# Optimization experiments

Hardware: AMD Instinct MI355X
Metric: run time of the kernel (lower is better)

Reference implementation:

```python
import jax, jax.numpy as jnp
import numpy as np

N_NODES = 50000
N_EDGES = 500000
CLIP_DIM = 512   # openai/clip-vit-base-patch32 projection_dim
HIDDEN = 512
NUM_CLASSES = 100


def setup_inputs() -> dict:
    key = jax.random.key(0)
    ks = jax.random.split(key, 8)
    x = jax.random.normal(ks[0], (N_NODES, CLIP_DIM), dtype=jnp.float32)
    edge_index = jax.random.randint(ks[1], (2, N_EDGES), 0, N_NODES)
    W1 = jax.random.normal(ks[2], (HIDDEN, CLIP_DIM), dtype=jnp.float32) / np.sqrt(CLIP_DIM)
    b1 = jnp.zeros((HIDDEN,), dtype=jnp.float32)
    W2 = jax.random.normal(ks[3], (HIDDEN, HIDDEN), dtype=jnp.float32) / np.sqrt(HIDDEN)
    b2 = jnp.zeros((HIDDEN,), dtype=jnp.float32)
    Wc = jax.random.normal(ks[4], (NUM_CLASSES, HIDDEN), dtype=jnp.float32) / np.sqrt(HIDDEN)
    bc = jnp.zeros((NUM_CLASSES,), dtype=jnp.float32)
    return {"x": x, "edge_index": edge_index, "W1": W1, "b1": b1,
            "W2": W2, "b2": b2, "Wc": Wc, "bc": bc}


def _gcn_conv(h, W, b, src, dst, coef, n_nodes):
    # PyG GCNConv: transform, then normalized scatter-add aggregation, then bias.
    h = h @ W.T                                   # [N, out]
    msg = h[src] * coef[:, None]                  # [E+N, out] gathered messages
    out = jax.ops.segment_sum(msg, dst, num_segments=n_nodes)
    return out + b


def reference(x, edge_index, W1, b1, W2, b2, Wc, bc):
    n = x.shape[0]
    loop = jnp.arange(n, dtype=edge_index.dtype)
    src = jnp.concatenate([edge_index[0], loop])  # add self-loops (GCN default)
    dst = jnp.concatenate([edge_index[1], loop])
    # symmetric normalization deg^-1/2 on both endpoints (unit edge weights)
    deg = jax.ops.segment_sum(jnp.ones_like(src, dtype=x.dtype), dst, num_segments=n)
    norm = jax.lax.rsqrt(deg)                     # deg >= 1 due to self-loops
    coef = norm[src] * norm[dst]

    h = _gcn_conv(x, W1, b1, src, dst, coef, n)
    h = jax.nn.relu(h)
    # dropout(p=0.2) is identity in eval mode
    h = _gcn_conv(h, W2, b2, src, dst, coef, n)
    h = jax.nn.relu(h)
    return h @ Wc.T + bc                          # [N, num_classes]
```

## Files before the change

### kernel.cpp

```cpp
#include <hip/hip_runtime.h>

#define HIDDEN 512
#define BLK_ELEMS (64 * 128 * 8)

typedef __attribute__((ext_vector_type(8))) short short8;
typedef __attribute__((ext_vector_type(4))) float f32x4;

__device__ __forceinline__ unsigned short f2bf(float f) {
    unsigned u = __float_as_uint(f);
    unsigned r = (u + 0x7FFFu + ((u >> 16) & 1u)) >> 16;
    return (unsigned short)r;
}
__device__ __forceinline__ float bf2f(unsigned short h) {
    return __uint_as_float(((unsigned)h) << 16);
}

__device__ __forceinline__ void load_lds16(const unsigned short* g, unsigned short* l) {
    __builtin_amdgcn_global_load_lds(
        (const __attribute__((address_space(1))) unsigned int*)(g),
        (__attribute__((address_space(3))) unsigned int*)(l), 16, 0, 0);
}

__device__ __forceinline__ void acc8(uint4 v, float cf, float* a) {
    a[0] = fmaf(cf, bf2f((unsigned short)(v.x & 0xFFFF)), a[0]);
    a[1] = fmaf(cf, bf2f((unsigned short)(v.x >> 16)),    a[1]);
    a[2] = fmaf(cf, bf2f((unsigned short)(v.y & 0xFFFF)), a[2]);
    a[3] = fmaf(cf, bf2f((unsigned short)(v.y >> 16)),    a[3]);
    a[4] = fmaf(cf, bf2f((unsigned short)(v.z & 0xFFFF)), a[4]);
    a[5] = fmaf(cf, bf2f((unsigned short)(v.z >> 16)),    a[5]);
    a[6] = fmaf(cf, bf2f((unsigned short)(v.w & 0xFFFF)), a[6]);
    a[7] = fmaf(cf, bf2f((unsigned short)(v.w >> 16)),    a[7]);
}


__device__ __forceinline__ void cast_chunk(const float* __restrict__ src,
                                           unsigned short* __restrict__ dst,
                                           int rows, int o) {
    int blk = o >> 13;
    int rem = o & 8191;
    int g = rem >> 7;
    int m = rem & 127;
    int row = blk * 128 + m;
    short8 v;
    if (row < rows) {
        const float* p = src + (size_t)row * HIDDEN + g * 8;
        float4 f0 = *(const float4*)p;
        float4 f1 = *(const float4*)(p + 4);
        v[0] = (short)f2bf(f0.x); v[1] = (short)f2bf(f0.y);
        v[2] = (short)f2bf(f0.z); v[3] = (short)f2bf(f0.w);
        v[4] = (short)f2bf(f1.x); v[5] = (short)f2bf(f1.y);
        v[6] = (short)f2bf(f1.z); v[7] = (short)f2bf(f1.w);
    } else {
        v = (short8)0;
    }
    *(short8*)(dst + (size_t)o * 8) = v;
}


__global__ __launch_bounds__(256)
void fused_count_castx(const int* __restrict__ dstv, int* __restrict__ cnt, int E, int countB,
                       const float* __restrict__ x, unsigned short* __restrict__ bufA,
                       int rows, int nxb) {
    int b = blockIdx.x;
    if (b < countB) {
        int e = b * 256 + threadIdx.x;
        if (e < E) atomicAdd(&cnt[dstv[e]], 1);
        return;
    }
    int cb = b - countB;
    if (cb >= nxb) return;
    __shared__ __align__(16) unsigned short xs[32 * 520];
    const int tid = threadIdx.x;
    const int r0 = cb * 32;
    #pragma unroll
    for (int p = 0; p < 16; ++p) {
        int f = p * 1024 + tid * 4;
        int rl = f >> 9;
        int col = f & 511;
        int grow = r0 + rl;
        uint2 w = make_uint2(0u, 0u);
        if (grow < rows) {
            float4 v = *(const float4*)(x + (size_t)grow * HIDDEN + col);
            w.x = (unsigned)f2bf(v.x) | ((unsigned)f2bf(v.y) << 16);
            w.y = (unsigned)f2bf(v.z) | ((unsigned)f2bf(v.w) << 16);
        }
        *(uint2*)(xs + rl * 520 + col) = w;
    }
    __syncthreads();
    const int blk = r0 >> 7;
    const int m0 = r0 & 127;
    unsigned short* dstb = bufA + (size_t)blk * BLK_ELEMS;
    #pragma unroll
    for (int p = 0; p < 8; ++p) {
        int c = p * 256 + tid;
        int g = c >> 5;
        int mloc = c & 31;
        short8 v = *(const short8*)(xs + mloc * 520 + g * 8);
        *(short8*)(dstb + g * 1024 + (m0 + mloc) * 8) = v;
    }
}


__global__ __launch_bounds__(256)
void fused_bsum_castw(const int* __restrict__ cnt, float* __restrict__ norm,
                      int* __restrict__ bsums, int n, int NSB,
                      const float* __restrict__ W1, const float* __restrict__ W2,
                      const float* __restrict__ Wc,
                      unsigned short* __restrict__ W1t, unsigned short* __restrict__ W2t,
                      unsigned short* __restrict__ Wct, int NC) {
    __shared__ int red[256];
    int tid = threadIdx.x;
    if ((int)blockIdx.x < NSB) {
        int i = blockIdx.x * 256 + tid;
        int v = 0;
        if (i < n) {
            v = cnt[i];
            norm[i] = rsqrtf((float)(v + 1));
        }
        red[tid] = v;
        __syncthreads();
        #pragma unroll
        for (int off = 128; off > 0; off >>= 1) {
            if (tid < off) red[tid] += red[tid + off];
            __syncthreads();
        }
        if (tid == 0) bsums[blockIdx.x] = red[0];
    } else {
        int o = ((int)blockIdx.x - NSB) * 256 + tid;
        if (o < 32768) {
            cast_chunk(W1, W1t, HIDDEN, o);
        } else if (o < 65536) {
            cast_chunk(W2, W2t, HIDDEN, o - 32768);
        } else if (o < 73728) {
            cast_chunk(Wc, Wct, NC, o - 65536);
        }
    }
}

__global__ __launch_bounds__(256)
void bscan_kernel(const int* __restrict__ bsums, int* __restrict__ boffs,
                  int* __restrict__ rowptr_n, int nb) {
    __shared__ int buf[256];
    int tid = threadIdx.x;
    int v = (tid < nb) ? bsums[tid] : 0;
    buf[tid] = v;
    __syncthreads();
    #pragma unroll
    for (int off = 1; off < 256; off <<= 1) {
        int t = (tid >= off) ? buf[tid - off] : 0;
        __syncthreads();
        buf[tid] += t;
        __syncthreads();
    }
    if (tid < nb) boffs[tid] = buf[tid] - v;
    if (tid == 255) rowptr_n[0] = buf[255];
}

__global__ __launch_bounds__(256)
void scan_final_kernel(const int* __restrict__ cnt, const int* __restrict__ boffs,
                       int* __restrict__ rowptr, int* __restrict__ cursor, int n) {
    __shared__ int buf[256];
    int tid = threadIdx.x;
    int i = blockIdx.x * 256 + tid;
    int v = (i < n) ? cnt[i] : 0;
    buf[tid] = v;
    __syncthreads();
    #pragma unroll
    for (int off = 1; off < 256; off <<= 1) {
        int t = (tid >= off) ? buf[tid - off] : 0;
        __syncthreads();
        buf[tid] += t;
        __syncthreads();
    }
    if (i < n) {
        int ex = boffs[blockIdx.x] + buf[tid] - v;
        rowptr[i] = ex;
        cursor[i] = ex;
    }
}


template<int MODE>
__device__ __forceinline__ void gemm_body(const unsigned short* __restrict__ At,
                                          const unsigned short* __restrict__ Bt,
                                          const float* __restrict__ bias,
                                          void* __restrict__ Cout,
                                          int M, int NC, int mb, int nb) {
    __shared__ __align__(16) unsigned short As[8 * 128 * 8];
    __shared__ __align__(16) unsigned short Bs[8 * 128 * 8];

    const int tid = threadIdx.x;
    const int wid = tid >> 6;
    const int lane = tid & 63;
    const int wm = wid & 1, wn = wid >> 1;
    const int lm = lane & 15;
    const int lq = lane >> 4;

    const unsigned short* Ab = At + (size_t)mb * BLK_ELEMS;
    const unsigned short* Bb = Bt + (size_t)nb * BLK_ELEMS;

    f32x4 acc[4][4];
    #pragma unroll
    for (int i = 0; i < 4; ++i)
        #pragma unroll
        for (int j = 0; j < 4; ++j) acc[i][j] = (f32x4)0.f;

    for (int kt = 0; kt < 8; ++kt) {
        __syncthreads();
        const unsigned short* ga = Ab + kt * (8 * 1024);
        const unsigned short* gb = Bb + kt * (8 * 1024);
        #pragma unroll
        for (int i = 0; i < 4; ++i) {
            int off = (tid + i * 256) * 8;
            load_lds16(ga + off, As + off);
            load_lds16(gb + off, Bs + off);
        }
        __syncthreads();
        #pragma unroll
        for (int ks = 0; ks < 2; ++ks) {
            int g = ks * 4 + lq;
            int base = g * 1024 + lm * 8;
            short8 af[4], bfr[4];
            #pragma unroll
            for (int mt = 0; mt < 4; ++mt)
                af[mt] = *(const short8*)&As[base + (wm * 64 + mt * 16) * 8];
            #pragma unroll
            for (int nt = 0; nt < 4; ++nt)
                bfr[nt] = *(const short8*)&Bs[base + (wn * 64 + nt * 16) * 8];
            #pragma unroll
            for (int mt = 0; mt < 4; ++mt)
                #pragma unroll
                for (int nt = 0; nt < 4; ++nt)
                    acc[mt][nt] = __builtin_amdgcn_mfma_f32_16x16x32_bf16(
                        af[mt], bfr[nt], acc[mt][nt], 0, 0, 0);
        }
    }

    #pragma unroll
    for (int mt = 0; mt < 4; ++mt) {
        #pragma unroll
        for (int nt = 0; nt < 4; ++nt) {
            int col = nb * 128 + wn * 64 + nt * 16 + lm;
            f32x4 v = acc[mt][nt];
            #pragma unroll
            for (int r = 0; r < 4; ++r) {
                int row = mb * 128 + wm * 64 + mt * 16 + lq * 4 + r;
                if (row < M) {
                    if (MODE == 0) {
                        ((unsigned short*)Cout)[(size_t)row * HIDDEN + col] = f2bf(v[r]);
                    } else {
                        if (col < NC)
                            ((float*)Cout)[(size_t)row * NC + col] = v[r] + bias[col];
                    }
                }
            }
        }
    }
}

__device__ __forceinline__ bool swz_decode(int bid, int NB, int& mb, int& nb) {
    int p = bid & 7;
    int s = bid >> 3;
    nb = s & 3;
    mb = (s >> 2) * 8 + p;
    return mb < NB;
}

template<int MODE>
__global__ __launch_bounds__(256)
void gemm_swz(const unsigned short* __restrict__ At, const unsigned short* __restrict__ Bt,
              const float* __restrict__ bias, void* __restrict__ Cout,
              int M, int NC, int NB) {
    int mb, nb;
    if (!swz_decode(blockIdx.x, NB, mb, nb)) return;
    gemm_body<MODE>(At, Bt, bias, Cout, M, NC, mb, nb);
}

template<int MODE>
__global__ __launch_bounds__(256)
void gemm_plain(const unsigned short* __restrict__ At, const unsigned short* __restrict__ Bt,
                const float* __restrict__ bias, void* __restrict__ Cout,
                int M, int NC) {
    gemm_body<MODE>(At, Bt, bias, Cout, M, NC, blockIdx.x, blockIdx.y);
}


__global__ __launch_bounds__(256)
void fused_fill_gemm1(const int* __restrict__ src, const int* __restrict__ dstv,
                      const float* __restrict__ norm, int* __restrict__ cursor,
                      int2* __restrict__ epair, int E, int fillB,
                      const unsigned short* __restrict__ At, const unsigned short* __restrict__ Bt,
                      void* __restrict__ Cout, int M, int NB) {
    int b = blockIdx.x;
    if (b < fillB) {
        int e = b * 256 + threadIdx.x;
        if (e < E) {
            int s = src[e], d = dstv[e];
            float cf = norm[s] * norm[d];
            int p = atomicAdd(&cursor[d], 1);
            epair[p] = make_int2(s, __float_as_int(cf));
        }
    } else {
        int mb, nb;
        if (swz_decode(b - fillB, NB, mb, nb))
            gemm_body<0>(At, Bt, nullptr, Cout, M, HIDDEN, mb, nb);
    }
}


__global__ __launch_bounds__(1024)
void aggregate_kernel(const unsigned short* __restrict__ h, const int* __restrict__ rowptr,
                      const int2* __restrict__ epair, const float* __restrict__ norm,
                      const float* __restrict__ bias, unsigned short* __restrict__ out_t,
                      int N) {
    const int wave = threadIdx.x >> 6;
    const int lane = threadIdx.x & 63;
    const int node = blockIdx.x * 16 + wave;
    if (node >= N) return;
    const uint4* h4 = (const uint4*)h;
    const int c = lane;

    float a[8];
    {
        uint4 sv = h4[(size_t)node * 64 + c];
        float nv = norm[node];
        float invd = nv * nv;
        a[0] = a[1] = a[2] = a[3] = a[4] = a[5] = a[6] = a[7] = 0.f;
        acc8(sv, invd, a);
    }

    int beg = rowptr[node], end = rowptr[node + 1];
    int j = beg;
    for (; j + 4 <= end; j += 4) {
        int2 p0 = epair[j + 0];
        int2 p1 = epair[j + 1];
        int2 p2 = epair[j + 2];
        int2 p3 = epair[j + 3];
        uint4 v0 = h4[(size_t)p0.x * 64 + c];
        uint4 v1 = h4[(size_t)p1.x * 64 + c];
        uint4 v2 = h4[(size_t)p2.x * 64 + c];
        uint4 v3 = h4[(size_t)p3.x * 64 + c];
        acc8(v0, __int_as_float(p0.y), a);
        acc8(v1, __int_as_float(p1.y), a);
        acc8(v2, __int_as_float(p2.y), a);
        acc8(v3, __int_as_float(p3.y), a);
    }
    for (; j < end; ++j) {
        int2 p = epair[j];
        uint4 v = h4[(size_t)p.x * 64 + c];
        acc8(v, __int_as_float(p.y), a);
    }

    const float4 b0 = *(const float4*)(bias + c * 8);
    const float4 b1 = *(const float4*)(bias + c * 8 + 4);
    a[0] = fmaxf(a[0] + b0.x, 0.f); a[1] = fmaxf(a[1] + b0.y, 0.f);
    a[2] = fmaxf(a[2] + b0.z, 0.f); a[3] = fmaxf(a[3] + b0.w, 0.f);
    a[4] = fmaxf(a[4] + b1.x, 0.f); a[5] = fmaxf(a[5] + b1.y, 0.f);
    a[6] = fmaxf(a[6] + b1.z, 0.f); a[7] = fmaxf(a[7] + b1.w, 0.f);

    size_t off = (size_t)(node >> 7) * BLK_ELEMS + (size_t)c * 1024 + (node & 127) * 8;
    uint4 o;
    o.x = (unsigned)f2bf(a[0]) | ((unsigned)f2bf(a[1]) << 16);
    o.y = (unsigned)f2bf(a[2]) | ((unsigned)f2bf(a[3]) << 16);
    o.z = (unsigned)f2bf(a[4]) | ((unsigned)f2bf(a[5]) << 16);
    o.w = (unsigned)f2bf(a[6]) | ((unsigned)f2bf(a[7]) << 16);
    *(uint4*)(out_t + off) = o;
}


extern "C" void kernel_launch(void* const* d_in, const int* in_sizes, int n_in,
                              void* d_out, int out_size, void* d_ws, size_t ws_size,
                              hipStream_t stream) {
    const float* x  = (const float*)d_in[0];
    const int*   ei = (const int*)d_in[1];
    const float* W1 = (const float*)d_in[2];
    const float* b1 = (const float*)d_in[3];
    const float* W2 = (const float*)d_in[4];
    const float* b2 = (const float*)d_in[5];
    const float* Wc = (const float*)d_in[6];
    const float* bc = (const float*)d_in[7];

    const int N  = in_sizes[0] / HIDDEN;
    const int E  = in_sizes[1] / 2;
    const int NC = in_sizes[6] / HIDDEN;
    const int NB = (N + 127) / 128;
    const int NSB = (N + 255) / 256;

    const int* src = ei;
    const int* dst = ei + E;

    char* ws = (char*)d_ws;
    int*   cnt    = (int*)(ws);
    int*   rowptr = (int*)(ws + (256 << 10));
    int*   cursor = (int*)(ws + (512 << 10));
    float* normv  = (float*)(ws + (768 << 10));
    int*   bsums  = (int*)(ws + (968 << 10));
    int*   boffs  = (int*)(ws + (990 << 10));
    int2*  epair  = (int2*)(ws + (1ull << 20));
    unsigned short* W1t = (unsigned short*)(ws + (6ull << 20));
    unsigned short* W2t = (unsigned short*)(ws + (6ull << 20) + (512 << 10));
    unsigned short* Wct = (unsigned short*)(ws + (7ull << 20));
    unsigned short* bufA = (unsigned short*)(ws + (16ull << 20));
    unsigned short* bufB = (unsigned short*)(ws + (80ull << 20));
    unsigned short* hbuf = (unsigned short*)(ws + (144ull << 20));

    const int countB = (E + 255) / 256;
    const int nxb = NB * 4;
    const int gemmB = 8 * 4 * ((NB + 7) / 8);

    hipMemsetAsync(cnt, 0, N * sizeof(int), stream);
    fused_count_castx<<<countB + nxb, 256, 0, stream>>>(dst, cnt, E, countB,
                                                        x, bufA, N, nxb);
    fused_bsum_castw<<<NSB + 288, 256, 0, stream>>>(cnt, normv, bsums, N, NSB,
                                                    W1, W2, Wc, W1t, W2t, Wct, NC);
    bscan_kernel<<<1, 256, 0, stream>>>(bsums, boffs, rowptr + N, NSB);
    scan_final_kernel<<<NSB, 256, 0, stream>>>(cnt, boffs, rowptr, cursor, N);
    fused_fill_gemm1<<<countB + gemmB, 256, 0, stream>>>(src, dst, normv, cursor, epair,
                                                         E, countB,
                                                         bufA, W1t, hbuf, N, NB);
    const int aggB = (N + 15) / 16;
    aggregate_kernel<<<aggB, 1024, 0, stream>>>(hbuf, rowptr, epair, normv, b1, bufB, N);
    gemm_swz<0><<<gemmB, 256, 0, stream>>>(bufB, W2t, nullptr, hbuf, N, HIDDEN, NB);
    aggregate_kernel<<<aggB, 1024, 0, stream>>>(hbuf, rowptr, epair, normv, b2, bufA, N);
    gemm_plain<1><<<dim3(NB, 1), 256, 0, stream>>>(bufA, Wct, bc, d_out, N, NC);
}
```

Before: 486.4 us.

## Use 256x256 tile GEMM with double-buffered LDS for second layer

Replaces the 128x128-tile GEMM for the second GCN transform with a new 512-thread kernel computing 256x256 output tiles. A and B blocks are staged via global_load_lds into double-buffered LDS, so the next K-step loads overlap with the MFMA work. The larger tile is meant to cut global and LDS traffic per FLOP and the number of workgroups. In exchange it needs 128 KB of LDS and 128 accumulator registers per thread, which lowers occupancy and leaves fewer blocks to spread across the CUs.

```diff
diff --git a/kernel.cpp b/kernel.cpp
--- a/kernel.cpp
+++ b/kernel.cpp
@@ -268,16 +268,6 @@
 
 template<int MODE>
 __global__ __launch_bounds__(256)
-void gemm_swz(const unsigned short* __restrict__ At, const unsigned short* __restrict__ Bt,
-              const float* __restrict__ bias, void* __restrict__ Cout,
-              int M, int NC, int NB) {
-    int mb, nb;
-    if (!swz_decode(blockIdx.x, NB, mb, nb)) return;
-    gemm_body<MODE>(At, Bt, bias, Cout, M, NC, mb, nb);
-}
-
-template<int MODE>
-__global__ __launch_bounds__(256)
 void gemm_plain(const unsigned short* __restrict__ At, const unsigned short* __restrict__ Bt,
                 const float* __restrict__ bias, void* __restrict__ Cout,
                 int M, int NC) {
@@ -304,6 +294,101 @@
         int mb, nb;
         if (swz_decode(b - fillB, NB, mb, nb))
             gemm_body<0>(At, Bt, nullptr, Cout, M, HIDDEN, mb, nb);
+    }
+}
+
+
+__device__ __forceinline__ void stage256(const unsigned short* __restrict__ At, size_t aBase,
+                                         const unsigned short* __restrict__ Bt, size_t bBase,
+                                         int kt, unsigned short* dst, int tid) {
+    #pragma unroll
+    for (int i = 0; i < 4; ++i) {
+        int f = i * 4096 + tid * 8;
+        int sl = f >> 13;
+        int rem = f & 8191;
+        load_lds16(At + aBase + (size_t)sl * BLK_ELEMS + (size_t)kt * 8192 + rem, dst + f);
+        load_lds16(Bt + bBase + (size_t)sl * BLK_ELEMS + (size_t)kt * 8192 + rem, dst + 16384 + f);
+    }
+}
+
+__global__ __launch_bounds__(512)
+void gemm256_swz(const unsigned short* __restrict__ At, const unsigned short* __restrict__ Bt,
+                 unsigned short* __restrict__ Cout, int M, int MB2) {
+    int p = blockIdx.x & 7;
+    int s = blockIdx.x >> 3;
+    int nb = s & 1;
+    int mb = (s >> 1) * 8 + p;
+    if (mb >= MB2) return;
+
+    __shared__ __align__(16) unsigned short lds[2 * 32768];
+
+    const int tid = threadIdx.x;
+    const int wid = tid >> 6;
+    const int lane = tid & 63;
+    const int wm = wid & 1;
+    const int wn = wid >> 1;
+    const int lm = lane & 15;
+    const int lq = lane >> 4;
+
+    const size_t aBase = (size_t)(2 * mb) * BLK_ELEMS;
+    const size_t bBase = (size_t)(2 * nb) * BLK_ELEMS;
+
+    f32x4 acc[8][4];
+    #pragma unroll
+    for (int i = 0; i < 8; ++i)
+        #pragma unroll
+        for (int j = 0; j < 4; ++j) acc[i][j] = (f32x4)0.f;
+
+    stage256(At, aBase, Bt, bBase, 0, lds, tid);
+
+    for (int kt = 0; kt < 8; ++kt) {
+        const int cur = kt & 1;
+        if (kt < 7) {
+            stage256(At, aBase, Bt, bBase, kt + 1, lds + (cur ^ 1) * 32768, tid);
+            asm volatile("s_waitcnt vmcnt(8)" ::: "memory");
+        } else {
+            asm volatile("s_waitcnt vmcnt(0)" ::: "memory");
+        }
+        asm volatile("s_barrier" ::: "memory");
+
+        const unsigned short* As = lds + cur * 32768;
+        const unsigned short* Bs = As + 16384;
+        __builtin_amdgcn_s_setprio(1);
+        #pragma unroll
+        for (int ks = 0; ks < 2; ++ks) {
+            const int g = ks * 4 + lq;
+            short8 bfr[4];
+            #pragma unroll
+            for (int nt = 0; nt < 4; ++nt) {
+                int cc = (wn & 1) * 64 + nt * 16 + lm;
+                bfr[nt] = *(const short8*)&Bs[(wn >> 1) * 8192 + g * 1024 + cc * 8];
+            }
+            #pragma unroll
+            for (int mt = 0; mt < 8; ++mt) {
+                short8 af = *(const short8*)&As[wm * 8192 + g * 1024 + (mt * 16 + lm) * 8];
+                #pragma unroll
+                for (int nt = 0; nt < 4; ++nt)
+                    acc[mt][nt] = __builtin_amdgcn_mfma_f32_16x16x32_bf16(
+                        af, bfr[nt], acc[mt][nt], 0, 0, 0);
+            }
+        }
+        __builtin_amdgcn_s_setprio(0);
+        asm volatile("s_barrier" ::: "memory");
+    }
+
+    #pragma unroll
+    for (int mt = 0; mt < 8; ++mt) {
+        #pragma unroll
+        for (int nt = 0; nt < 4; ++nt) {
+            int col = nb * 256 + wn * 64 + nt * 16 + lm;
+            f32x4 v = acc[mt][nt];
+            #pragma unroll
+            for (int r = 0; r < 4; ++r) {
+                int row = mb * 256 + wm * 128 + mt * 16 + lq * 4 + r;
+                if (row < M)
+                    Cout[(size_t)row * HIDDEN + col] = f2bf(v[r]);
+            }
+        }
     }
 }
 
@@ -385,6 +470,7 @@
     const int NC = in_sizes[6] / HIDDEN;
     const int NB = (N + 127) / 128;
     const int NSB = (N + 255) / 256;
+    const int MB2 = (N + 255) / 256;
 
     const int* src = ei;
     const int* dst = ei + E;
@@ -407,6 +493,7 @@
     const int countB = (E + 255) / 256;
     const int nxb = NB * 4;
     const int gemmB = 8 * 4 * ((NB + 7) / 8);
+    const int gemm2B = 8 * 2 * ((MB2 + 7) / 8);
 
     hipMemsetAsync(cnt, 0, N * sizeof(int), stream);
     fused_count_castx<<<countB + nxb, 256, 0, stream>>>(dst, cnt, E, countB,
@@ -420,7 +507,7 @@
                                                          bufA, W1t, hbuf, N, NB);
     const int aggB = (N + 15) / 16;
     aggregate_kernel<<<aggB, 1024, 0, stream>>>(hbuf, rowptr, epair, normv, b1, bufB, N);
-    gemm_swz<0><<<gemmB, 256, 0, stream>>>(bufB, W2t, nullptr, hbuf, N, HIDDEN, NB);
+    gemm256_swz<<<gemm2B, 512, 0, stream>>>(bufB, W2t, hbuf, N, MB2);
     aggregate_kernel<<<aggB, 1024, 0, stream>>>(hbuf, rowptr, epair, normv, b2, bufA, N);
     gemm_plain<1><<<dim3(NB, 1), 256, 0, stream>>>(bufA, Wct, bc, d_out, N, NC);
 }
```

New measurement: 492.7 us. No clear change (+1.3%).

## Fuse classifier into second aggregation and merge block-sum scan into final scan

Applied to the files above, without the earlier changes.

The second GCN aggregation now computes the 100-class classifier in the same kernel. Each wave dots its aggregated 512-wide node row against bf16 classifier weights and reduces across lanes with xor shuffles, so the bf16 hidden buffer is never written and reread and the separate MFMA classifier GEMM is gone. The single-block scan of block sums is folded into the final scan kernel, where each block re-scans the block sums itself, removing one launch. The cost is that the classifier moves from matrix cores to scalar FMAs plus many cross-lane shuffles per node, which may cost more than the memory traffic and launch it saves.

```diff
diff --git a/kernel.cpp b/kernel.cpp
--- a/kernel.cpp
+++ b/kernel.cpp
@@ -137,12 +137,16 @@
     }
 }
 
+
 __global__ __launch_bounds__(256)
-void bscan_kernel(const int* __restrict__ bsums, int* __restrict__ boffs,
-                  int* __restrict__ rowptr_n, int nb) {
+void scan_final_kernel(const int* __restrict__ cnt, const int* __restrict__ bsums,
+                       int* __restrict__ rowptr, int* __restrict__ cursor,
+                       int n, int NSB) {
     __shared__ int buf[256];
-    int tid = threadIdx.x;
-    int v = (tid < nb) ? bsums[tid] : 0;
+    __shared__ int base;
+    const int tid = threadIdx.x;
+    const int b = blockIdx.x;
+    int v = (tid < NSB) ? bsums[tid] : 0;
     buf[tid] = v;
     __syncthreads();
     #pragma unroll
@@ -152,18 +156,12 @@
         buf[tid] += t;
         __syncthreads();
     }
-    if (tid < nb) boffs[tid] = buf[tid] - v;
-    if (tid == 255) rowptr_n[0] = buf[255];
-}
-
-__global__ __launch_bounds__(256)
-void scan_final_kernel(const int* __restrict__ cnt, const int* __restrict__ boffs,
-                       int* __restrict__ rowptr, int* __restrict__ cursor, int n) {
-    __shared__ int buf[256];
-    int tid = threadIdx.x;
-    int i = blockIdx.x * 256 + tid;
-    int v = (i < n) ? cnt[i] : 0;
-    buf[tid] = v;
+    if (tid == 0) base = (b > 0) ? buf[b - 1] : 0;
+    if (b == 0 && tid == 0) rowptr[n] = buf[255];
+    __syncthreads();
+    int i = b * 256 + tid;
+    int c = (i < n) ? cnt[i] : 0;
+    buf[tid] = c;
     __syncthreads();
     #pragma unroll
     for (int off = 1; off < 256; off <<= 1) {
@@ -173,19 +171,17 @@
         __syncthreads();
     }
     if (i < n) {
-        int ex = boffs[blockIdx.x] + buf[tid] - v;
+        int ex = base + buf[tid] - c;
         rowptr[i] = ex;
         cursor[i] = ex;
     }
 }
 
 
-template<int MODE>
 __device__ __forceinline__ void gemm_body(const unsigned short* __restrict__ At,
                                           const unsigned short* __restrict__ Bt,
-                                          const float* __restrict__ bias,
                                           void* __restrict__ Cout,
-                                          int M, int NC, int mb, int nb) {
+                                          int M, int mb, int nb) {
     __shared__ __align__(16) unsigned short As[8 * 128 * 8];
     __shared__ __align__(16) unsigned short Bs[8 * 128 * 8];
 
@@ -245,14 +241,8 @@
             #pragma unroll
             for (int r = 0; r < 4; ++r) {
                 int row = mb * 128 + wm * 64 + mt * 16 + lq * 4 + r;
-                if (row < M) {
-                    if (MODE == 0) {
-                        ((unsigned short*)Cout)[(size_t)row * HIDDEN + col] = f2bf(v[r]);
-                    } else {
-                        if (col < NC)
-                            ((float*)Cout)[(size_t)row * NC + col] = v[r] + bias[col];
-                    }
-                }
+                if (row < M)
+                    ((unsigned short*)Cout)[(size_t)row * HIDDEN + col] = f2bf(v[r]);
             }
         }
     }
@@ -266,22 +256,12 @@
     return mb < NB;
 }
 
-template<int MODE>
 __global__ __launch_bounds__(256)
 void gemm_swz(const unsigned short* __restrict__ At, const unsigned short* __restrict__ Bt,
-              const float* __restrict__ bias, void* __restrict__ Cout,
-              int M, int NC, int NB) {
+              void* __restrict__ Cout, int M, int NB) {
     int mb, nb;
     if (!swz_decode(blockIdx.x, NB, mb, nb)) return;
-    gemm_body<MODE>(At, Bt, bias, Cout, M, NC, mb, nb);
-}
-
-template<int MODE>
-__global__ __launch_bounds__(256)
-void gemm_plain(const unsigned short* __restrict__ At, const unsigned short* __restrict__ Bt,
-                const float* __restrict__ bias, void* __restrict__ Cout,
-                int M, int NC) {
-    gemm_body<MODE>(At, Bt, bias, Cout, M, NC, blockIdx.x, blockIdx.y);
+    gemm_body(At, Bt, Cout, M, mb, nb);
 }
 
 
@@ -303,7 +283,7 @@
     } else {
         int mb, nb;
         if (swz_decode(b - fillB, NB, mb, nb))
-            gemm_body<0>(At, Bt, nullptr, Cout, M, HIDDEN, mb, nb);
+            gemm_body(At, Bt, Cout, M, mb, nb);
     }
 }
 
@@ -368,6 +348,132 @@
 }
 
 
+__global__ __launch_bounds__(1024)
+void aggregate_cls_kernel(const unsigned short* __restrict__ h, const int* __restrict__ rowptr,
+                          const int2* __restrict__ epair, const float* __restrict__ norm,
+                          const float* __restrict__ bias, const unsigned short* __restrict__ Wct,
+                          const float* __restrict__ bc, float* __restrict__ out,
+                          int N, int NC) {
+    const int wave = threadIdx.x >> 6;
+    const int lane = threadIdx.x & 63;
+    const int node = blockIdx.x * 16 + wave;
+    if (node >= N) return;
+    const uint4* h4 = (const uint4*)h;
+    const int c = lane;
+
+    float a[8];
+    {
+        uint4 sv = h4[(size_t)node * 64 + c];
+        float nv = norm[node];
+        float invd = nv * nv;
+        a[0] = a[1] = a[2] = a[3] = a[4] = a[5] = a[6] = a[7] = 0.f;
+        acc8(sv, invd, a);
+    }
+
+    int beg = rowptr[node], end = rowptr[node + 1];
+    int j = beg;
+    for (; j + 4 <= end; j += 4) {
+        int2 p0 = epair[j + 0];
+        int2 p1 = epair[j + 1];
+        int2 p2 = epair[j + 2];
+        int2 p3 = epair[j + 3];
+        uint4 v0 = h4[(size_t)p0.x * 64 + c];
+        uint4 v1 = h4[(size_t)p1.x * 64 + c];
+        uint4 v2 = h4[(size_t)p2.x * 64 + c];
+        uint4 v3 = h4[(size_t)p3.x * 64 + c];
+        acc8(v0, __int_as_float(p0.y), a);
+        acc8(v1, __int_as_float(p1.y), a);
+        acc8(v2, __int_as_float(p2.y), a);
+        acc8(v3, __int_as_float(p3.y), a);
+    }
+    for (; j < end; ++j) {
+        int2 p = epair[j];
+        uint4 v = h4[(size_t)p.x * 64 + c];
+        acc8(v, __int_as_float(p.y), a);
+    }
+
+    const float4 b0 = *(const float4*)(bias + c * 8);
+    const float4 b1 = *(const float4*)(bias + c * 8 + 4);
+    a[0] = fmaxf(a[0] + b0.x, 0.f); a[1] = fmaxf(a[1] + b0.y, 0.f);
+    a[2] = fmaxf(a[2] + b0.z, 0.f); a[3] = fmaxf(a[3] + b0.w, 0.f);
+    a[4] = fmaxf(a[4] + b1.x, 0.f); a[5] = fmaxf(a[5] + b1.y, 0.f);
+    a[6] = fmaxf(a[6] + b1.z, 0.f); a[7] = fmaxf(a[7] + b1.w, 0.f);
+
+    const unsigned short* wc = Wct + (size_t)c * 1024;
+    float* po = out + (size_t)node * NC;
+    int k = 0;
+    for (; k + 4 <= NC; k += 4) {
+        float p0, p1, p2, p3;
+        {
+            uint4 w0 = *(const uint4*)(wc + (k + 0) * 8);
+            uint4 w1 = *(const uint4*)(wc + (k + 1) * 8);
+            uint4 w2 = *(const uint4*)(wc + (k + 2) * 8);
+            uint4 w3 = *(const uint4*)(wc + (k + 3) * 8);
+            p0 = a[0] * bf2f((unsigned short)(w0.x & 0xFFFF));
+            p1 = a[0] * bf2f((unsigned short)(w1.x & 0xFFFF));
+            p2 = a[0] * bf2f((unsigned short)(w2.x & 0xFFFF));
+            p3 = a[0] * bf2f((unsigned short)(w3.x & 0xFFFF));
+            p0 = fmaf(a[1], bf2f((unsigned short)(w0.x >> 16)), p0);
+            p1 = fmaf(a[1], bf2f((unsigned short)(w1.x >> 16)), p1);
+            p2 = fmaf(a[1], bf2f((unsigned short)(w2.x >> 16)), p2);
+            p3 = fmaf(a[1], bf2f((unsigned short)(w3.x >> 16)), p3);
+            p0 = fmaf(a[2], bf2f((unsigned short)(w0.y & 0xFFFF)), p0);
+            p1 = fmaf(a[2], bf2f((unsigned short)(w1.y & 0xFFFF)), p1);
+            p2 = fmaf(a[2], bf2f((unsigned short)(w2.y & 0xFFFF)), p2);
+            p3 = fmaf(a[2], bf2f((unsigned short)(w3.y & 0xFFFF)), p3);
+            p0 = fmaf(a[3], bf2f((unsigned short)(w0.y >> 16)), p0);
+            p1 = fmaf(a[3], bf2f((unsigned short)(w1.y >> 16)), p1);
+            p2 = fmaf(a[3], bf2f((unsigned short)(w2.y >> 16)), p2);
+            p3 = fmaf(a[3], bf2f((unsigned short)(w3.y >> 16)), p3);
+            p0 = fmaf(a[4], bf2f((unsigned short)(w0.z & 0xFFFF)), p0);
+            p1 = fmaf(a[4], bf2f((unsigned short)(w1.z & 0xFFFF)), p1);
+            p2 = fmaf(a[4], bf2f((unsigned short)(w2.z & 0xFFFF)), p2);
+            p3 = fmaf(a[4], bf2f((unsigned short)(w3.z & 0xFFFF)), p3);
+            p0 = fmaf(a[5], bf2f((unsigned short)(w0.z >> 16)), p0);
+            p1 = fmaf(a[5], bf2f((unsigned short)(w1.z >> 16)), p1);
+            p2 = fmaf(a[5], bf2f((unsigned short)(w2.z >> 16)), p2);
+            p3 = fmaf(a[5], bf2f((unsigned short)(w3.z >> 16)), p3);
+            p0 = fmaf(a[6], bf2f((unsigned short)(w0.w & 0xFFFF)), p0);
+            p1 = fmaf(a[6], bf2f((unsigned short)(w1.w & 0xFFFF)), p1);
+            p2 = fmaf(a[6], bf2f((unsigned short)(w2.w & 0xFFFF)), p2);
+            p3 = fmaf(a[6], bf2f((unsigned short)(w3.w & 0xFFFF)), p3);
+            p0 = fmaf(a[7], bf2f((unsigned short)(w0.w >> 16)), p0);
+            p1 = fmaf(a[7], bf2f((unsigned short)(w1.w >> 16)), p1);
+            p2 = fmaf(a[7], bf2f((unsigned short)(w2.w >> 16)), p2);
+            p3 = fmaf(a[7], bf2f((unsigned short)(w3.w >> 16)), p3);
+        }
+        #pragma unroll
+        for (int m = 1; m < 64; m <<= 1) {
+            p0 += __shfl_xor(p0, m);
+            p1 += __shfl_xor(p1, m);
+            p2 += __shfl_xor(p2, m);
+            p3 += __shfl_xor(p3, m);
+        }
+        if (lane == 0) {
+            po[k + 0] = p0 + bc[k + 0];
+            po[k + 1] = p1 + bc[k + 1];
+            po[k + 2] = p2 + bc[k + 2];
+            po[k + 3] = p3 + bc[k + 3];
+        }
+    }
+    for (; k < NC; ++k) {
+        uint4 w0 = *(const uint4*)(wc + k * 8);
+        float p0;
+        p0 = a[0] * bf2f((unsigned short)(w0.x & 0xFFFF));
+        p0 = fmaf(a[1], bf2f((unsigned short)(w0.x >> 16)), p0);
+        p0 = fmaf(a[2], bf2f((unsigned short)(w0.y & 0xFFFF)), p0);
+        p0 = fmaf(a[3], bf2f((unsigned short)(w0.y >> 16)), p0);
+        p0 = fmaf(a[4], bf2f((unsigned short)(w0.z & 0xFFFF)), p0);
+        p0 = fmaf(a[5], bf2f((unsigned short)(w0.z >> 16)), p0);
+        p0 = fmaf(a[6], bf2f((unsigned short)(w0.w & 0xFFFF)), p0);
+        p0 = fmaf(a[7], bf2f((unsigned short)(w0.w >> 16)), p0);
+        #pragma unroll
+        for (int m = 1; m < 64; m <<= 1) p0 += __shfl_xor(p0, m);
+        if (lane == 0) po[k] = p0 + bc[k];
+    }
+}
+
+
 extern "C" void kernel_launch(void* const* d_in, const int* in_sizes, int n_in,
                               void* d_out, int out_size, void* d_ws, size_t ws_size,
                               hipStream_t stream) {
@@ -395,7 +501,6 @@
     int*   cursor = (int*)(ws + (512 << 10));
     float* normv  = (float*)(ws + (768 << 10));
     int*   bsums  = (int*)(ws + (968 << 10));
-    int*   boffs  = (int*)(ws + (990 << 10));
     int2*  epair  = (int2*)(ws + (1ull << 20));
     unsigned short* W1t = (unsigned short*)(ws + (6ull << 20));
     unsigned short* W2t = (unsigned short*)(ws + (6ull << 20) + (512 << 10));
@@ -413,14 +518,13 @@
                                                         x, bufA, N, nxb);
     fused_bsum_castw<<<NSB + 288, 256, 0, stream>>>(cnt, normv, bsums, N, NSB,
                                                     W1, W2, Wc, W1t, W2t, Wct, NC);
-    bscan_kernel<<<1, 256, 0, stream>>>(bsums, boffs, rowptr + N, NSB);
-    scan_final_kernel<<<NSB, 256, 0, stream>>>(cnt, boffs, rowptr, cursor, N);
+    scan_final_kernel<<<NSB, 256, 0, stream>>>(cnt, bsums, rowptr, cursor, N, NSB);
     fused_fill_gemm1<<<countB + gemmB, 256, 0, stream>>>(src, dst, normv, cursor, epair,
                                                          E, countB,
                                                          bufA, W1t, hbuf, N, NB);
     const int aggB = (N + 15) / 16;
     aggregate_kernel<<<aggB, 1024, 0, stream>>>(hbuf, rowptr, epair, normv, b1, bufB, N);
-    gemm_swz<0><<<gemmB, 256, 0, stream>>>(bufB, W2t, nullptr, hbuf, N, HIDDEN, NB);
-    aggregate_kernel<<<aggB, 1024, 0, stream>>>(hbuf, rowptr, epair, normv, b2, bufA, N);
-    gemm_plain<1><<<dim3(NB, 1), 256, 0, stream>>>(bufA, Wct, bc, d_out, N, NC);
-}
+    gemm_swz<<<gemmB, 256, 0, stream>>>(bufB, W2t, hbuf, N, NB);
+    aggregate_cls_kernel<<<aggB, 1024, 0, stream>>>(hbuf, rowptr, epair, normv, b2,
+                                                    Wct, bc, (float*)d_out, N, NC);
+}
```

Result: slower. 1.039 ms (+113.5%).
